# Kernel optimization log

Hardware: AMD Instinct MI355X
Metric: run time of the kernel (lower is better)

## Reference

```python
import jax, jax.numpy as jnp
import numpy as np

# Emformer config (from torchaudio.models.Emformer in BasicNet4)
D, H, FFN, L = 512, 4, 128, 4      # input_dim, num_heads, ffn_dim, num_layers
SEG, RC = 4, 1                     # segment_length, right_context_length
B, T = 8, 1025
U = T - RC                         # utterance length = 1024
NSEG = -(-U // SEG)                # 256 segments
R = NSEG * RC                      # total right-context frames = 256
DH = D // H


def _right_context_indices():
    # torchaudio _gen_right_context: segment i's right context = frames [(i+1)*SEG : (i+1)*SEG+RC],
    # last block = input[T-RC:]
    idx = [np.arange((i + 1) * SEG, (i + 1) * SEG + RC) for i in range(NSEG - 1)]
    idx.append(np.arange(T - RC, T))
    return np.concatenate(idx)


def _attention_mask():
    # Rows / cols ordered [right-context blocks (seg order), utterance frames].
    # A query belonging to segment i may attend to segment i's right-context block
    # and segment i's utterance frames (left_context_length=0, no memory bank).
    seg_rc = np.repeat(np.arange(NSEG), RC)
    seg_u = np.arange(U) // SEG
    seg_q = np.concatenate([seg_rc, seg_u])
    seg_k = np.concatenate([seg_rc, seg_u])
    return seg_q[:, None] == seg_k[None, :]  # (R+U, R+U), True = allowed


def _ln(x, g, b, eps=1e-5):
    mu = jnp.mean(x, -1, keepdims=True)
    var = jnp.mean(jnp.square(x - mu), -1, keepdims=True)
    return (x - mu) * jax.lax.rsqrt(var + eps) * g + b


def setup_inputs() -> dict:
    key = jax.random.key(0)
    ks = jax.random.split(key, 8)
    s = 0.02
    return {
        "x": jax.random.normal(ks[0], (B, T, D), jnp.float32),
        "Wq": jax.random.normal(ks[1], (L, D, D), jnp.float32) * s,
        "bq": jnp.zeros((L, D), jnp.float32),
        "Wkv": jax.random.normal(ks[2], (L, 2 * D, D), jnp.float32) * s,
        "bkv": jnp.zeros((L, 2 * D), jnp.float32),
        "Wo": jax.random.normal(ks[3], (L, D, D), jnp.float32) * s,
        "bo": jnp.zeros((L, D), jnp.float32),
        "W1": jax.random.normal(ks[4], (L, FFN, D), jnp.float32) * s,
        "b1": jnp.zeros((L, FFN), jnp.float32),
        "W2": jax.random.normal(ks[5], (L, D, FFN), jnp.float32) * s,
        "b2": jnp.zeros((L, D), jnp.float32),
        "ln_in_g": jnp.ones((L, D), jnp.float32),
        "ln_in_b": jnp.zeros((L, D), jnp.float32),
        "ff_ln_g": jnp.ones((L, D), jnp.float32),
        "ff_ln_b": jnp.zeros((L, D), jnp.float32),
        "ln_out_g": jnp.ones((L, D), jnp.float32),
        "ln_out_b": jnp.zeros((L, D), jnp.float32),
    }


def reference(x, Wq, bq, Wkv, bkv, Wo, bo, W1, b1, W2, b2,
              ln_in_g, ln_in_b, ff_ln_g, ff_ln_b, ln_out_g, ln_out_b):
    rc_idx = jnp.asarray(_right_context_indices())
    allowed = jnp.asarray(_attention_mask())
    scale = DH ** -0.5
    u = x[:, :U]          # (B, U, D) utterance
    r = x[:, rc_idx]      # (B, R, D) gathered right-context blocks
    for l in range(L):
        cat = jnp.concatenate([r, u], axis=1)            # (B, R+U, D)
        ln = _ln(cat, ln_in_g[l], ln_in_b[l])            # pre-attention LN
        q = (ln @ Wq[l].T + bq[l]).reshape(B, R + U, H, DH)
        kv = ln @ Wkv[l].T + bkv[l]
        k = kv[..., :D].reshape(B, R + U, H, DH)
        v = kv[..., D:].reshape(B, R + U, H, DH)
        scores = jnp.einsum("bqhd,bkhd->bhqk", q * scale, k)
        scores = jnp.where(allowed, scores, -jnp.inf)
        probs = jax.nn.softmax(scores, axis=-1)
        attn = jnp.einsum("bhqk,bkhd->bqhd", probs, v).reshape(B, R + U, D)
        rc_out = attn @ Wo[l].T + bo[l] + cat            # residual w/ pre-LN input
        h = _ln(rc_out, ff_ln_g[l], ff_ln_b[l])
        h = jax.nn.relu(h @ W1[l].T + b1[l]) @ W2[l].T + b2[l]
        rc_out = _ln(rc_out + h, ln_out_g[l], ln_out_b[l])
        r, u = rc_out[:, :R], rc_out[:, R:]
    return u.mean(axis=1)  # (B, D): mean-pool over utterance frames
```

## Files before the change

### kernel.cpp

```cpp
#include <hip/hip_runtime.h>
#include <cstdint>
#include <cstddef>

#define D_    512
#define H_    4
#define DH_   128
#define FFN_  128
#define L_    4
#define B_    8
#define T_    1025
#define U_    1024
#define NSEG_ 256
#define R_    256
#define TOT_  1280
#define M_    (B_*TOT_)
#define CH_   1536

typedef __attribute__((ext_vector_type(8))) short bf16x8;
typedef __attribute__((ext_vector_type(4))) float f32x4;
typedef unsigned short u16;

__device__ __forceinline__ u16 f2bf(float f) {
  unsigned u = __builtin_bit_cast(unsigned, f);
  u += 0x7fff + ((u >> 16) & 1);
  return (u16)(u >> 16);
}
__device__ __forceinline__ float bf2f(u16 h) {
  unsigned u = ((unsigned)h) << 16;
  return __builtin_bit_cast(float, u);
}

__device__ __forceinline__ void gload_lds16(const void* g, void* l) {
  __builtin_amdgcn_global_load_lds(
      (const __attribute__((address_space(1))) unsigned*)g,
      (__attribute__((address_space(3))) unsigned*)l, 16, 0, 0);
}

__global__ __launch_bounds__(256)
void cvt_all_k(const float* __restrict__ Wq, const float* __restrict__ Wkv,
               const float* __restrict__ Wo, const float* __restrict__ W1,
               const float* __restrict__ W2, const float* __restrict__ bq,
               const float* __restrict__ bkv,
               u16* __restrict__ WQKVb, u16* __restrict__ Wob,
               u16* __restrict__ W1b, u16* __restrict__ W2b,
               float* __restrict__ bQKV) {
  int i4 = blockIdx.x * 256 + threadIdx.x;
  if (i4 < 786432) {
    int e = i4 * 4;
    int l = e / 786432;
    int rem = e - l * 786432;
    int n = rem >> 9, k = rem & 511;
    const float* src = (n < 512) ? (Wq + (size_t)l * 262144 + n * 512 + k)
                                 : (Wkv + (size_t)l * 524288 + (n - 512) * 512 + k);
    float4 v = *(const float4*)src;
    ushort4 o; o.x = f2bf(v.x); o.y = f2bf(v.y); o.z = f2bf(v.z); o.w = f2bf(v.w);
    *(ushort4*)(WQKVb + e) = o;
  } else if (i4 < 1048576) {
    int e = (i4 - 786432) * 4;
    float4 v = *(const float4*)(Wo + e);
    ushort4 o; o.x = f2bf(v.x); o.y = f2bf(v.y); o.z = f2bf(v.z); o.w = f2bf(v.w);
    *(ushort4*)(Wob + e) = o;
  } else if (i4 < 1114112) {
    int e = (i4 - 1048576) * 4;
    float4 v = *(const float4*)(W1 + e);
    ushort4 o; o.x = f2bf(v.x); o.y = f2bf(v.y); o.z = f2bf(v.z); o.w = f2bf(v.w);
    *(ushort4*)(W1b + e) = o;
  } else if (i4 < 1179648) {
    int e = (i4 - 1114112) * 4;
    float4 v = *(const float4*)(W2 + e);
    ushort4 o; o.x = f2bf(v.x); o.y = f2bf(v.y); o.z = f2bf(v.z); o.w = f2bf(v.w);
    *(ushort4*)(W2b + e) = o;
  } else if (i4 < 1181184) {
    int e = (i4 - 1179648) * 4;
    int l = e / 1536, n = e - l * 1536;
#pragma unroll
    for (int t = 0; t < 4; ++t) {
      int nn = n + t;
      bQKV[e + t] = (nn < 512) ? bq[l * 512 + nn] : bkv[l * 1024 + (nn - 512)];
    }
  }
}

__global__ __launch_bounds__(256)
void gather_ln_k(const float* __restrict__ x, const float* __restrict__ g,
                 const float* __restrict__ bb, float* __restrict__ X,
                 u16* __restrict__ LNb) {
  int row = blockIdx.x;
  int tid = threadIdx.x;
  int b = row / TOT_, p = row % TOT_;
  int t = (p < R_) ? ((p < R_ - 1) ? 4 * (p + 1) : (T_ - 1)) : (p - R_);
  const float* xr = x + ((size_t)b * T_ + t) * D_;
  float e0 = xr[tid], e1 = xr[tid + 256];
  X[(size_t)row * D_ + tid] = e0;
  X[(size_t)row * D_ + tid + 256] = e1;
  float s = e0 + e1, ss = e0 * e0 + e1 * e1;
#pragma unroll
  for (int off = 32; off > 0; off >>= 1) {
    s  += __shfl_down(s, off);
    ss += __shfl_down(ss, off);
  }
  __shared__ float red[10];
  int wid = tid >> 6, lane = tid & 63;
  if (lane == 0) { red[wid] = s; red[4 + wid] = ss; }
  __syncthreads();
  if (tid == 0) {
    float S = red[0] + red[1] + red[2] + red[3];
    float SS = red[4] + red[5] + red[6] + red[7];
    float mu = S * (1.0f / D_);
    float var = SS * (1.0f / D_) - mu * mu;
    if (var < 0.f) var = 0.f;
    red[8] = mu; red[9] = rsqrtf(var + 1e-5f);
  }
  __syncthreads();
  float mu = red[8], rs = red[9];
  u16* yr = LNb + (size_t)row * D_;
  yr[tid]       = f2bf((e0 - mu) * rs * g[tid]       + bb[tid]);
  yr[tid + 256] = f2bf((e1 - mu) * rs * g[tid + 256] + bb[tid + 256]);
}

#define GBK 32

__global__ __launch_bounds__(256)
void gemm_qkv(const u16* __restrict__ A, const u16* __restrict__ Bw,
              const float* __restrict__ bias, u16* __restrict__ Cout) {
  __shared__ __align__(16) u16 As[128 * GBK];
  __shared__ __align__(16) u16 Bs[128 * GBK];
  const int tid = threadIdx.x;
  const int wid = tid >> 6;
  const int lane = tid & 63;
  const int bid = blockIdx.x;
  const int xcd = bid & 7;
  const int t = bid >> 3;
  const int cb = t % 12;
  const int rb = xcd * 10 + t / 12;
  const int bm = rb * 128;
  const int bn = cb * 128;
  const int wr = wid >> 1, wc = wid & 1;

  const int srow = tid >> 2;
  const int skoff = (tid & 3) << 3;

  f32x4 acc[4][4] = {};

  const u16* Ag0 = A  + (size_t)(bm + srow)      * D_ + skoff;
  const u16* Ag1 = A  + (size_t)(bm + 64 + srow) * D_ + skoff;
  const u16* Bg0 = Bw + (size_t)(bn + srow)      * D_ + skoff;
  const u16* Bg1 = Bw + (size_t)(bn + 64 + srow) * D_ + skoff;
  u16* AsW0 = &As[(size_t)(wid * 16)      * GBK];
  u16* AsW1 = &As[(size_t)(64 + wid * 16) * GBK];
  u16* BsW0 = &Bs[(size_t)(wid * 16)      * GBK];
  u16* BsW1 = &Bs[(size_t)(64 + wid * 16) * GBK];

  const int lrow = lane & 15;
  const int lko  = (lane >> 4) * 16;

  for (int k0 = 0; k0 < D_; k0 += GBK) {
    __syncthreads();
    gload_lds16(Ag0 + k0, AsW0);
    gload_lds16(Ag1 + k0, AsW1);
    gload_lds16(Bg0 + k0, BsW0);
    gload_lds16(Bg1 + k0, BsW1);
    __syncthreads();

    bf16x8 afrag[4], bfrag[4];
#pragma unroll
    for (int m = 0; m < 4; ++m) {
      int row = wr * 64 + m * 16 + lrow;
      afrag[m] = *(const bf16x8*)((const char*)As + row * (GBK * 2) + lko);
    }
#pragma unroll
    for (int n = 0; n < 4; ++n) {
      int col = wc * 64 + n * 16 + lrow;
      bfrag[n] = *(const bf16x8*)((const char*)Bs + col * (GBK * 2) + lko);
    }
#pragma unroll
    for (int m = 0; m < 4; ++m)
#pragma unroll
      for (int n = 0; n < 4; ++n)
        acc[m][n] = __builtin_amdgcn_mfma_f32_16x16x32_bf16(
            afrag[m], bfrag[n], acc[m][n], 0, 0, 0);
  }

  const int lcol  = lane & 15;
  const int lrow4 = (lane >> 4) * 4;
#pragma unroll
  for (int m = 0; m < 4; ++m) {
    int rowbase = bm + wr * 64 + m * 16 + lrow4;
#pragma unroll
    for (int n = 0; n < 4; ++n) {
      int col = bn + wc * 64 + n * 16 + lcol;
      float bv = bias[col];
#pragma unroll
      for (int j = 0; j < 4; ++j) {
        int row = rowbase + j;
        Cout[(size_t)row * CH_ + col] = f2bf(acc[m][n][j] + bv);
      }
    }
  }
}

template <int MODE>
__global__ __launch_bounds__(256)
void gemm_row_ln(const u16* __restrict__ A, const u16* __restrict__ Bw,
                 const float* __restrict__ bias, const float* __restrict__ Rsd,
                 float* __restrict__ Xout,
                 const float* __restrict__ g1, const float* __restrict__ b1,
                 const float* __restrict__ g2, const float* __restrict__ b2,
                 u16* __restrict__ OutBf, int K) {
  __shared__ __align__(16) u16 As[16 * 32];
  __shared__ __align__(16) u16 Bs[512 * 32];
  __shared__ float wsum[4][16], wss[4][16], mu_s[16], rs_s[16];
  const int tid = threadIdx.x;
  const int wid = tid >> 6, lane = tid & 63;
  const int bm = blockIdx.x * 16;
  const int l4 = lane >> 2;
  const int k8 = (lane & 3) << 3;
  const int lrow = lane & 15;
  const int lko  = (lane >> 4) * 16;

  f32x4 acc[8] = {};

  const u16* Ag = A + (size_t)(bm + l4) * K + k8;

  for (int k0 = 0; k0 < K; k0 += 32) {
    __syncthreads();
    if (wid == 0)
      gload_lds16(Ag + k0, As);
#pragma unroll
    for (int p = 0; p < 8; ++p) {
      int row = wid * 128 + p * 16 + l4;
      gload_lds16(Bw + (size_t)row * K + k0 + k8,
                  (char*)Bs + (wid * 128 + p * 16) * 64);
    }
    __syncthreads();

    bf16x8 af = *(const bf16x8*)((const char*)As + lrow * 64 + lko);
    bf16x8 bf[8];
#pragma unroll
    for (int n = 0; n < 8; ++n)
      bf[n] = *(const bf16x8*)((const char*)Bs + (wid * 128 + n * 16 + lrow) * 64 + lko);
#pragma unroll
    for (int n = 0; n < 8; ++n)
      acc[n] = __builtin_amdgcn_mfma_f32_16x16x32_bf16(af, bf[n], acc[n], 0, 0, 0);
  }

  const int lcol = lane & 15;
  const int lr4 = (lane >> 4) * 4;
#pragma unroll
  for (int n = 0; n < 8; ++n) {
    int col = wid * 128 + n * 16 + lcol;
    float bv = bias[col];
#pragma unroll
    for (int j = 0; j < 4; ++j) {
      int row = bm + lr4 + j;
      float t = acc[n][j] + bv + Rsd[(size_t)row * D_ + col];
      if (MODE == 0) Xout[(size_t)row * D_ + col] = t;
      acc[n][j] = t;
    }
  }

  {
    float s0[4] = {}, s1[4] = {};
#pragma unroll
    for (int n = 0; n < 8; ++n)
#pragma unroll
      for (int j = 0; j < 4; ++j) {
        float v = acc[n][j];
        s0[j] += v; s1[j] += v * v;
      }
#pragma unroll
    for (int off = 1; off < 16; off <<= 1)
#pragma unroll
      for (int j = 0; j < 4; ++j) {
        s0[j] += __shfl_xor(s0[j], off);
        s1[j] += __shfl_xor(s1[j], off);
      }
    if ((lane & 15) == 0) {
#pragma unroll
      for (int j = 0; j < 4; ++j) {
        wsum[wid][lr4 + j] = s0[j]; wss[wid][lr4 + j] = s1[j];
      }
    }
  }
  __syncthreads();
  if (tid < 16) {
    float S  = wsum[0][tid] + wsum[1][tid] + wsum[2][tid] + wsum[3][tid];
    float SS = wss[0][tid] + wss[1][tid] + wss[2][tid] + wss[3][tid];
    float mu = S * (1.0f / D_);
    float var = SS * (1.0f / D_) - mu * mu;
    if (var < 0.f) var = 0.f;
    mu_s[tid] = mu; rs_s[tid] = rsqrtf(var + 1e-5f);
  }
  __syncthreads();

  float gg[8], bv2[8];
#pragma unroll
  for (int n = 0; n < 8; ++n) {
    int col = wid * 128 + n * 16 + lcol;
    gg[n] = g1[col]; bv2[n] = b1[col];
  }
#pragma unroll
  for (int n = 0; n < 8; ++n) {
    int col = wid * 128 + n * 16 + lcol;
#pragma unroll
    for (int j = 0; j < 4; ++j) {
      int r = lr4 + j;
      int row = bm + r;
      float ln = (acc[n][j] - mu_s[r]) * rs_s[r] * gg[n] + bv2[n];
      if (MODE == 0) {
        OutBf[(size_t)row * D_ + col] = f2bf(ln);
      } else {
        Xout[(size_t)row * D_ + col] = ln;
        acc[n][j] = ln;
      }
    }
  }

  if (MODE == 1) {
    __syncthreads();
    {
      float s0[4] = {}, s1[4] = {};
#pragma unroll
      for (int n = 0; n < 8; ++n)
#pragma unroll
        for (int j = 0; j < 4; ++j) {
          float v = acc[n][j];
          s0[j] += v; s1[j] += v * v;
        }
#pragma unroll
      for (int off = 1; off < 16; off <<= 1)
#pragma unroll
        for (int j = 0; j < 4; ++j) {
          s0[j] += __shfl_xor(s0[j], off);
          s1[j] += __shfl_xor(s1[j], off);
        }
      if ((lane & 15) == 0) {
#pragma unroll
        for (int j = 0; j < 4; ++j) {
          wsum[wid][lr4 + j] = s0[j]; wss[wid][lr4 + j] = s1[j];
        }
      }
    }
    __syncthreads();
    if (tid < 16) {
      float S  = wsum[0][tid] + wsum[1][tid] + wsum[2][tid] + wsum[3][tid];
      float SS = wss[0][tid] + wss[1][tid] + wss[2][tid] + wss[3][tid];
      float mu = S * (1.0f / D_);
      float var = SS * (1.0f / D_) - mu * mu;
      if (var < 0.f) var = 0.f;
      mu_s[tid] = mu; rs_s[tid] = rsqrtf(var + 1e-5f);
    }
    __syncthreads();
#pragma unroll
    for (int n = 0; n < 8; ++n) {
      int col = wid * 128 + n * 16 + lcol;
      gg[n] = g2[col]; bv2[n] = b2[col];
    }
#pragma unroll
    for (int n = 0; n < 8; ++n) {
      int col = wid * 128 + n * 16 + lcol;
#pragma unroll
      for (int j = 0; j < 4; ++j) {
        int r = lr4 + j;
        int row = bm + r;
        float ln = (acc[n][j] - mu_s[r]) * rs_s[r] * gg[n] + bv2[n];
        OutBf[(size_t)row * D_ + col] = f2bf(ln);
      }
    }
  }
}

__global__ __launch_bounds__(256)
void gemm_ffn1(const u16* __restrict__ A, const u16* __restrict__ Bw,
               const float* __restrict__ bias, u16* __restrict__ Hout) {
  __shared__ __align__(16) u16 As[16 * 32];
  __shared__ __align__(16) u16 Bs[128 * 32];
  const int tid = threadIdx.x;
  const int wid = tid >> 6, lane = tid & 63;
  const int bm = blockIdx.x * 16;
  const int l4 = lane >> 2;
  const int k8 = (lane & 3) << 3;
  const int lrow = lane & 15;
  const int lko  = (lane >> 4) * 16;

  f32x4 acc[2] = {};
  const u16* Ag = A + (size_t)(bm + l4) * D_ + k8;

  for (int k0 = 0; k0 < D_; k0 += 32) {
    __syncthreads();
    if (wid == 0)
      gload_lds16(Ag + k0, As);
#pragma unroll
    for (int p = 0; p < 2; ++p) {
      int row = wid * 32 + p * 16 + l4;
      gload_lds16(Bw + (size_t)row * D_ + k0 + k8,
                  (char*)Bs + (wid * 32 + p * 16) * 64);
    }
    __syncthreads();
    bf16x8 af = *(const bf16x8*)((const char*)As + lrow * 64 + lko);
    bf16x8 bf[2];
#pragma unroll
    for (int n = 0; n < 2; ++n)
      bf[n] = *(const bf16x8*)((const char*)Bs + (wid * 32 + n * 16 + lrow) * 64 + lko);
#pragma unroll
    for (int n = 0; n < 2; ++n)
      acc[n] = __builtin_amdgcn_mfma_f32_16x16x32_bf16(af, bf[n], acc[n], 0, 0, 0);
  }

  const int lcol = lane & 15;
  const int lr4 = (lane >> 4) * 4;
#pragma unroll
  for (int n = 0; n < 2; ++n) {
    int col = wid * 32 + n * 16 + lcol;
    float bv = bias[col];
#pragma unroll
    for (int j = 0; j < 4; ++j) {
      int row = bm + lr4 + j;
      float v = fmaxf(acc[n][j] + bv, 0.f);
      Hout[(size_t)row * FFN_ + col] = f2bf(v);
    }
  }
}

#define QLD 516
__global__ __launch_bounds__(256)
void attn_k(const u16* __restrict__ QKV, u16* __restrict__ O) {
  int bs = blockIdx.x;
  int b = bs >> 8, s = bs & 255;
  __shared__ float Qs[5][QLD];
  __shared__ float Ks[5][QLD];
  __shared__ float Vs[5][QLD];
  __shared__ float P[H_][5][5];
  int tid = threadIdx.x;
  const float scale = 0.08838834764831845f;
  int rows[5];
  rows[0] = s;
#pragma unroll
  for (int i = 1; i < 5; ++i) rows[i] = R_ + 4 * s + (i - 1);
  for (int idx = tid; idx < 960; idx += 256) {
    int mtx = idx / 320;
    int rem = idx - mtx * 320;
    int i = rem >> 6, c8 = rem & 63;
    size_t base = ((size_t)b * TOT_ + rows[i]) * CH_ + mtx * 512 + c8 * 8;
    bf16x8 v = *(const bf16x8*)(QKV + base);
    float* dst = (mtx == 0) ? &Qs[i][c8 * 8] : (mtx == 1 ? &Ks[i][c8 * 8] : &Vs[i][c8 * 8]);
    if (mtx == 0) {
#pragma unroll
      for (int t = 0; t < 8; ++t) dst[t] = bf2f((u16)v[t]) * scale;
    } else {
#pragma unroll
      for (int t = 0; t < 8; ++t) dst[t] = bf2f((u16)v[t]);
    }
  }
  __syncthreads();
  int h = tid >> 6, lane = tid & 63;
  if (lane < 25) {
    int i = lane / 5, j = lane % 5;
    float sum = 0.f;
    const float* qp = &Qs[i][h * DH_];
    const float* kp = &Ks[j][h * DH_];
#pragma unroll 8
    for (int d = 0; d < DH_; ++d) sum += qp[d] * kp[d];
    P[h][i][j] = sum;
  }
  __syncthreads();
  if (lane < 5) {
    int i = lane;
    float m = P[h][i][0];
#pragma unroll
    for (int j = 1; j < 5; ++j) m = fmaxf(m, P[h][i][j]);
    float e[5], ssum = 0.f;
#pragma unroll
    for (int j = 0; j < 5; ++j) { e[j] = __expf(P[h][i][j] - m); ssum += e[j]; }
    float inv = 1.0f / ssum;
#pragma unroll
    for (int j = 0; j < 5; ++j) P[h][i][j] = e[j] * inv;
  }
  __syncthreads();
  for (int idx = lane; idx < 5 * DH_; idx += 64) {
    int i = idx >> 7, d = idx & (DH_ - 1);
    float o = 0.f;
#pragma unroll
    for (int j = 0; j < 5; ++j) o += P[h][i][j] * Vs[j][h * DH_ + d];
    O[((size_t)b * TOT_ + rows[i]) * D_ + h * DH_ + d] = f2bf(o);
  }
}

__global__ __launch_bounds__(256)
void mean_part_k(const float* __restrict__ X, float* __restrict__ part) {
  int d = blockIdx.x * 256 + threadIdx.x;
  int jc = blockIdx.y;
  int b = blockIdx.z;
  float acc = 0.f;
  const float* base = X + ((size_t)b * TOT_ + R_ + jc * 128) * D_ + d;
  for (int j = 0; j < 128; ++j) acc += base[(size_t)j * D_];
  part[((size_t)b * 8 + jc) * D_ + d] = acc;
}

__global__ __launch_bounds__(256)
void mean_final_k(const float* __restrict__ part, float* __restrict__ out) {
  int i = blockIdx.x * 256 + threadIdx.x;
  int b = i >> 9, d = i & (D_ - 1);
  float acc = 0.f;
#pragma unroll
  for (int c = 0; c < 8; ++c) acc += part[((size_t)b * 8 + c) * D_ + d];
  out[i] = acc * (1.0f / U_);
}

extern "C" void kernel_launch(void* const* d_in, const int* in_sizes, int n_in,
                              void* d_out, int out_size, void* d_ws, size_t ws_size,
                              hipStream_t stream) {
  const float* x      = (const float*)d_in[0];
  const float* Wq     = (const float*)d_in[1];
  const float* bq     = (const float*)d_in[2];
  const float* Wkv    = (const float*)d_in[3];
  const float* bkv    = (const float*)d_in[4];
  const float* Wo     = (const float*)d_in[5];
  const float* bo     = (const float*)d_in[6];
  const float* W1     = (const float*)d_in[7];
  const float* b1     = (const float*)d_in[8];
  const float* W2     = (const float*)d_in[9];
  const float* b2     = (const float*)d_in[10];
  const float* ln_in_g  = (const float*)d_in[11];
  const float* ln_in_b  = (const float*)d_in[12];
  const float* ff_ln_g  = (const float*)d_in[13];
  const float* ff_ln_b  = (const float*)d_in[14];
  const float* ln_out_g = (const float*)d_in[15];
  const float* ln_out_b = (const float*)d_in[16];
  float* out = (float*)d_out;

  char* wsb = (char*)d_ws;
  float* X     = (float*)wsb;
  u16*   LNbuf = (u16*)(wsb + 20971520);
  u16*   QKV   = (u16*)(wsb + 31457280);
  u16*   ATT   = (u16*)(wsb + 62914560);
  u16*   LN2b  = (u16*)(wsb + 73400320);
  u16*   Hb    = (u16*)(wsb + 83886080);
  float* part  = (float*)(wsb + 86507520);
  u16*   WQKVb = (u16*)(wsb + 86638592);
  u16*   Wob   = (u16*)(wsb + 92930048);
  u16*   W1b   = (u16*)(wsb + 95027200);
  u16*   W2b   = (u16*)(wsb + 95551488);
  float* bQKV  = (float*)(wsb + 96075776);

  cvt_all_k<<<4614, 256, 0, stream>>>(Wq, Wkv, Wo, W1, W2, bq, bkv,
                                      WQKVb, Wob, W1b, W2b, bQKV);
  gather_ln_k<<<M_, 256, 0, stream>>>(x, ln_in_g, ln_in_b, X, LNbuf);

  for (int l = 0; l < L_; ++l) {
    const u16* WQKV_l = WQKVb + (size_t)l * CH_ * D_;
    const u16* Wo_l   = Wob   + (size_t)l * D_ * D_;
    const u16* W1_l   = W1b   + (size_t)l * FFN_ * D_;
    const u16* W2_l   = W2b   + (size_t)l * D_ * FFN_;
    const float* bQKV_l = bQKV + (size_t)l * CH_;
    const float* bo_l = bo + (size_t)l * D_;
    const float* b1_l = b1 + (size_t)l * FFN_;
    const float* b2_l = b2 + (size_t)l * D_;

    gemm_qkv<<<960, 256, 0, stream>>>(LNbuf, WQKV_l, bQKV_l, QKV);

    attn_k<<<B_ * NSEG_, 256, 0, stream>>>(QKV, ATT);

    gemm_row_ln<0><<<M_ / 16, 256, 0, stream>>>(
        ATT, Wo_l, bo_l, X, X,
        ff_ln_g + l * D_, ff_ln_b + l * D_, nullptr, nullptr, LN2b, D_);

    gemm_ffn1<<<M_ / 16, 256, 0, stream>>>(LN2b, W1_l, b1_l, Hb);

    if (l < L_ - 1) {
      gemm_row_ln<1><<<M_ / 16, 256, 0, stream>>>(
          Hb, W2_l, b2_l, X, X,
          ln_out_g + l * D_, ln_out_b + l * D_,
          ln_in_g + (l + 1) * D_, ln_in_b + (l + 1) * D_, LNbuf, FFN_);
    } else {
      gemm_row_ln<2><<<M_ / 16, 256, 0, stream>>>(
          Hb, W2_l, b2_l, X, X,
          ln_out_g + l * D_, ln_out_b + l * D_,
          nullptr, nullptr, nullptr, FFN_);
    }
  }

  mean_part_k<<<dim3(2, 8, 8), 256, 0, stream>>>(X, part);
  mean_final_k<<<(B_ * D_) / 256, 256, 0, stream>>>(part, out);
}
```

Measured before the change: 438.6 us.

## Double-buffer LDS tiles and XOR-swizzle layout in QKV GEMM

Gives the QKV projection GEMM two LDS buffers so the global-to-LDS load of the next K tile is issued before the MFMA work on the current tile, and drops one of the two barriers per iteration. It also XOR-swizzles the 16-byte slot each row is stored in and read from, to reduce LDS bank conflicts on fragment reads. LDS use doubles, which may lower occupancy. Correctness relies on the write and read swizzles matching and on the single barrier being enough to order buffer reuse.

Result: no change. 446.3 us (+1.8%).

```diff
diff --git a/kernel.cpp b/kernel.cpp
--- a/kernel.cpp
+++ b/kernel.cpp
@@ -119,12 +119,13 @@
 }
 
 #define GBK 32
+#define QBUF (128 * GBK)
 
 __global__ __launch_bounds__(256)
 void gemm_qkv(const u16* __restrict__ A, const u16* __restrict__ Bw,
               const float* __restrict__ bias, u16* __restrict__ Cout) {
-  __shared__ __align__(16) u16 As[128 * GBK];
-  __shared__ __align__(16) u16 Bs[128 * GBK];
+  __shared__ __align__(16) u16 As[2 * QBUF];
+  __shared__ __align__(16) u16 Bs[2 * QBUF];
   const int tid = threadIdx.x;
   const int wid = tid >> 6;
   const int lane = tid & 63;
@@ -137,8 +138,9 @@
   const int bn = cb * 128;
   const int wr = wid >> 1, wc = wid & 1;
 
-  const int srow = tid >> 2;
-  const int skoff = (tid & 3) << 3;
+  const int srow  = tid >> 2;
+  const int sslot = (tid & 3) ^ ((tid >> 3) & 3);
+  const int skoff = sslot << 3;
 
   f32x4 acc[4][4] = {};
 
@@ -152,26 +154,37 @@
   u16* BsW1 = &Bs[(size_t)(64 + wid * 16) * GBK];
 
   const int lrow = lane & 15;
-  const int lko  = (lane >> 4) * 16;
-
+  const int lko  = (((lane >> 4) ^ ((lrow >> 1) & 3)) << 4);
+
+  gload_lds16(Ag0, AsW0);
+  gload_lds16(Ag1, AsW1);
+  gload_lds16(Bg0, BsW0);
+  gload_lds16(Bg1, BsW1);
+  __syncthreads();
+
+  int cur = 0;
+#pragma unroll 4
   for (int k0 = 0; k0 < D_; k0 += GBK) {
-    __syncthreads();
-    gload_lds16(Ag0 + k0, AsW0);
-    gload_lds16(Ag1 + k0, AsW1);
-    gload_lds16(Bg0 + k0, BsW0);
-    gload_lds16(Bg1 + k0, BsW1);
-    __syncthreads();
-
+    int nxt = cur ^ 1;
+    if (k0 + GBK < D_) {
+      gload_lds16(Ag0 + k0 + GBK, AsW0 + nxt * QBUF);
+      gload_lds16(Ag1 + k0 + GBK, AsW1 + nxt * QBUF);
+      gload_lds16(Bg0 + k0 + GBK, BsW0 + nxt * QBUF);
+      gload_lds16(Bg1 + k0 + GBK, BsW1 + nxt * QBUF);
+    }
+
+    const char* Ab = (const char*)(As + cur * QBUF);
+    const char* Bb = (const char*)(Bs + cur * QBUF);
     bf16x8 afrag[4], bfrag[4];
 #pragma unroll
     for (int m = 0; m < 4; ++m) {
       int row = wr * 64 + m * 16 + lrow;
-      afrag[m] = *(const bf16x8*)((const char*)As + row * (GBK * 2) + lko);
+      afrag[m] = *(const bf16x8*)(Ab + row * (GBK * 2) + lko);
     }
 #pragma unroll
     for (int n = 0; n < 4; ++n) {
       int col = wc * 64 + n * 16 + lrow;
-      bfrag[n] = *(const bf16x8*)((const char*)Bs + col * (GBK * 2) + lko);
+      bfrag[n] = *(const bf16x8*)(Bb + col * (GBK * 2) + lko);
     }
 #pragma unroll
     for (int m = 0; m < 4; ++m)
@@ -179,6 +192,9 @@
       for (int n = 0; n < 4; ++n)
         acc[m][n] = __builtin_amdgcn_mfma_f32_16x16x32_bf16(
             afrag[m], bfrag[n], acc[m][n], 0, 0, 0);
+
+    __syncthreads();
+    cur = nxt;
   }
 
   const int lcol  = lane & 15;
```

## Use 128x128 tiled O-proj GEMM and fuse FF LayerNorm into FFN1

Applied to the files above, without the earlier changes.

Replaces the 16-row, full-width O-projection kernel, which also computed the FF LayerNorm, with a 128x128-tiled GEMM using an XCD-aware block mapping. That kernel adds bias and residual in place into X. The FF LayerNorm moves into the FFN1 kernel: it reads the fp32 X rows, normalises them into a swizzled bf16 LDS tile, then runs the W1 GEMM. This is meant to improve weight reuse in the O-proj GEMM and drop the intermediate LN2 bf16 buffer. The cost is that FFN1 now re-reads the fp32 X and computes the LN statistics with a single-pass variance formula.

After: 400.5 us. 8.7% less time.

```diff
diff --git a/kernel.cpp b/kernel.cpp
--- a/kernel.cpp
+++ b/kernel.cpp
@@ -199,6 +199,175 @@
   }
 }
 
+__global__ __launch_bounds__(256)
+void gemm_oproj(const u16* __restrict__ A, const u16* __restrict__ Bw,
+                const float* __restrict__ bias, float* __restrict__ Xio) {
+  __shared__ __align__(16) u16 As[128 * GBK];
+  __shared__ __align__(16) u16 Bs[128 * GBK];
+  const int tid = threadIdx.x;
+  const int wid = tid >> 6;
+  const int lane = tid & 63;
+  const int bid = blockIdx.x;
+  const int xcd = bid & 7;
+  const int t = bid >> 3;
+  const int cb = t & 3;
+  const int rb = xcd * 10 + (t >> 2);
+  const int bm = rb * 128;
+  const int bn = cb * 128;
+  const int wr = wid >> 1, wc = wid & 1;
+
+  const int srow = tid >> 2;
+  const int skoff = (tid & 3) << 3;
+
+  f32x4 acc[4][4] = {};
+
+  const u16* Ag0 = A  + (size_t)(bm + srow)      * D_ + skoff;
+  const u16* Ag1 = A  + (size_t)(bm + 64 + srow) * D_ + skoff;
+  const u16* Bg0 = Bw + (size_t)(bn + srow)      * D_ + skoff;
+  const u16* Bg1 = Bw + (size_t)(bn + 64 + srow) * D_ + skoff;
+  u16* AsW0 = &As[(size_t)(wid * 16)      * GBK];
+  u16* AsW1 = &As[(size_t)(64 + wid * 16) * GBK];
+  u16* BsW0 = &Bs[(size_t)(wid * 16)      * GBK];
+  u16* BsW1 = &Bs[(size_t)(64 + wid * 16) * GBK];
+
+  const int lrow = lane & 15;
+  const int lko  = (lane >> 4) * 16;
+
+  for (int k0 = 0; k0 < D_; k0 += GBK) {
+    __syncthreads();
+    gload_lds16(Ag0 + k0, AsW0);
+    gload_lds16(Ag1 + k0, AsW1);
+    gload_lds16(Bg0 + k0, BsW0);
+    gload_lds16(Bg1 + k0, BsW1);
+    __syncthreads();
+
+    bf16x8 afrag[4], bfrag[4];
+#pragma unroll
+    for (int m = 0; m < 4; ++m) {
+      int row = wr * 64 + m * 16 + lrow;
+      afrag[m] = *(const bf16x8*)((const char*)As + row * (GBK * 2) + lko);
+    }
+#pragma unroll
+    for (int n = 0; n < 4; ++n) {
+      int col = wc * 64 + n * 16 + lrow;
+      bfrag[n] = *(const bf16x8*)((const char*)Bs + col * (GBK * 2) + lko);
+    }
+#pragma unroll
+    for (int m = 0; m < 4; ++m)
+#pragma unroll
+      for (int n = 0; n < 4; ++n)
+        acc[m][n] = __builtin_amdgcn_mfma_f32_16x16x32_bf16(
+            afrag[m], bfrag[n], acc[m][n], 0, 0, 0);
+  }
+
+  const int lcol  = lane & 15;
+  const int lrow4 = (lane >> 4) * 4;
+#pragma unroll
+  for (int m = 0; m < 4; ++m) {
+    int rowbase = bm + wr * 64 + m * 16 + lrow4;
+#pragma unroll
+    for (int n = 0; n < 4; ++n) {
+      int col = bn + wc * 64 + n * 16 + lcol;
+      float bv = bias[col];
+#pragma unroll
+      for (int j = 0; j < 4; ++j) {
+        size_t idx = (size_t)(rowbase + j) * D_ + col;
+        Xio[idx] = acc[m][n][j] + bv + Xio[idx];
+      }
+    }
+  }
+}
+
+__global__ __launch_bounds__(256)
+void ffn1_ln(const float* __restrict__ X,
+             const float* __restrict__ gff, const float* __restrict__ bff,
+             const u16* __restrict__ W1, const float* __restrict__ b1,
+             u16* __restrict__ Hout) {
+  __shared__ __align__(16) u16 Aln[16 * 512];
+  __shared__ __align__(16) u16 Bs[128 * 32];
+  const int tid = threadIdx.x;
+  const int wid = tid >> 6, lane = tid & 63;
+  const int bm = blockIdx.x * 16;
+  const int r  = tid >> 4;
+  const int jj = tid & 15;
+
+  const float* xr = X + (size_t)(bm + r) * D_ + jj * 32;
+  float v[32];
+  float s = 0.f, ss = 0.f;
+#pragma unroll
+  for (int i = 0; i < 8; ++i) {
+    float4 q = *(const float4*)(xr + i * 4);
+    v[i * 4 + 0] = q.x; v[i * 4 + 1] = q.y;
+    v[i * 4 + 2] = q.z; v[i * 4 + 3] = q.w;
+    s  += q.x + q.y + q.z + q.w;
+    ss += q.x * q.x + q.y * q.y + q.z * q.z + q.w * q.w;
+  }
+#pragma unroll
+  for (int off = 1; off < 16; off <<= 1) {
+    s  += __shfl_xor(s, off);
+    ss += __shfl_xor(ss, off);
+  }
+  float mu = s * (1.0f / D_);
+  float var = ss * (1.0f / D_) - mu * mu;
+  if (var < 0.f) var = 0.f;
+  float rs = rsqrtf(var + 1e-5f);
+
+  char* Ab = (char*)Aln;
+#pragma unroll
+  for (int i = 0; i < 8; ++i) {
+    int c0 = jj * 32 + i * 4;
+    float4 g4 = *(const float4*)(gff + c0);
+    float4 b4 = *(const float4*)(bff + c0);
+    ushort4 o;
+    o.x = f2bf((v[i * 4 + 0] - mu) * rs * g4.x + b4.x);
+    o.y = f2bf((v[i * 4 + 1] - mu) * rs * g4.y + b4.y);
+    o.z = f2bf((v[i * 4 + 2] - mu) * rs * g4.z + b4.z);
+    o.w = f2bf((v[i * 4 + 3] - mu) * rs * g4.w + b4.w);
+    int byteoff = (r * 1024 + c0 * 2) ^ ((r & 7) << 4);
+    *(ushort4*)(Ab + byteoff) = o;
+  }
+  __syncthreads();
+
+  const int lrow = lane & 15;
+  const int lko  = (lane >> 4) << 4;
+  const int l4 = lane >> 2;
+  const int k8 = (lane & 3) << 3;
+  f32x4 acc[2] = {};
+
+  for (int k0 = 0; k0 < D_; k0 += 32) {
+    if (k0) __syncthreads();
+#pragma unroll
+    for (int p = 0; p < 2; ++p) {
+      int rowb = wid * 32 + p * 16 + l4;
+      gload_lds16(W1 + (size_t)rowb * D_ + k0 + k8,
+                  (char*)Bs + (wid * 32 + p * 16) * 64);
+    }
+    __syncthreads();
+    bf16x8 af = *(const bf16x8*)((const char*)Aln +
+                  ((lrow * 1024 + k0 * 2 + lko) ^ ((lrow & 7) << 4)));
+    bf16x8 bf[2];
+#pragma unroll
+    for (int n = 0; n < 2; ++n)
+      bf[n] = *(const bf16x8*)((const char*)Bs + (wid * 32 + n * 16 + lrow) * 64 + lko);
+#pragma unroll
+    for (int n = 0; n < 2; ++n)
+      acc[n] = __builtin_amdgcn_mfma_f32_16x16x32_bf16(af, bf[n], acc[n], 0, 0, 0);
+  }
+
+  const int lcol = lane & 15;
+  const int lr4 = (lane >> 4) * 4;
+#pragma unroll
+  for (int n = 0; n < 2; ++n) {
+    int col = wid * 32 + n * 16 + lcol;
+    float bv = b1[col];
+#pragma unroll
+    for (int j = 0; j < 4; ++j) {
+      int row = bm + lr4 + j;
+      Hout[(size_t)row * FFN_ + col] = f2bf(fmaxf(acc[n][j] + bv, 0.f));
+    }
+  }
+}
+
 template <int MODE>
 __global__ __launch_bounds__(256)
 void gemm_row_ln(const u16* __restrict__ A, const u16* __restrict__ Bw,
@@ -254,7 +423,6 @@
     for (int j = 0; j < 4; ++j) {
       int row = bm + lr4 + j;
       float t = acc[n][j] + bv + Rsd[(size_t)row * D_ + col];
-      if (MODE == 0) Xout[(size_t)row * D_ + col] = t;
       acc[n][j] = t;
     }
   }
@@ -307,12 +475,8 @@
       int r = lr4 + j;
       int row = bm + r;
       float ln = (acc[n][j] - mu_s[r]) * rs_s[r] * gg[n] + bv2[n];
-      if (MODE == 0) {
-        OutBf[(size_t)row * D_ + col] = f2bf(ln);
-      } else {
-        Xout[(size_t)row * D_ + col] = ln;
-        acc[n][j] = ln;
-      }
+      Xout[(size_t)row * D_ + col] = ln;
+      acc[n][j] = ln;
     }
   }
 
@@ -366,58 +530,6 @@
         float ln = (acc[n][j] - mu_s[r]) * rs_s[r] * gg[n] + bv2[n];
         OutBf[(size_t)row * D_ + col] = f2bf(ln);
       }
-    }
-  }
-}
-
-__global__ __launch_bounds__(256)
-void gemm_ffn1(const u16* __restrict__ A, const u16* __restrict__ Bw,
-               const float* __restrict__ bias, u16* __restrict__ Hout) {
-  __shared__ __align__(16) u16 As[16 * 32];
-  __shared__ __align__(16) u16 Bs[128 * 32];
-  const int tid = threadIdx.x;
-  const int wid = tid >> 6, lane = tid & 63;
-  const int bm = blockIdx.x * 16;
-  const int l4 = lane >> 2;
-  const int k8 = (lane & 3) << 3;
-  const int lrow = lane & 15;
-  const int lko  = (lane >> 4) * 16;
-
-  f32x4 acc[2] = {};
-  const u16* Ag = A + (size_t)(bm + l4) * D_ + k8;
-
-  for (int k0 = 0; k0 < D_; k0 += 32) {
-    __syncthreads();
-    if (wid == 0)
-      gload_lds16(Ag + k0, As);
-#pragma unroll
-    for (int p = 0; p < 2; ++p) {
-      int row = wid * 32 + p * 16 + l4;
-      gload_lds16(Bw + (size_t)row * D_ + k0 + k8,
-                  (char*)Bs + (wid * 32 + p * 16) * 64);
-    }
-    __syncthreads();
-    bf16x8 af = *(const bf16x8*)((const char*)As + lrow * 64 + lko);
-    bf16x8 bf[2];
-#pragma unroll
-    for (int n = 0; n < 2; ++n)
-      bf[n] = *(const bf16x8*)((const char*)Bs + (wid * 32 + n * 16 + lrow) * 64 + lko);
-#pragma unroll
-    for (int n = 0; n < 2; ++n)
-      acc[n] = __builtin_amdgcn_mfma_f32_16x16x32_bf16(af, bf[n], acc[n], 0, 0, 0);
-  }
-
-  const int lcol = lane & 15;
-  const int lr4 = (lane >> 4) * 4;
-#pragma unroll
-  for (int n = 0; n < 2; ++n) {
-    int col = wid * 32 + n * 16 + lcol;
-    float bv = bias[col];
-#pragma unroll
-    for (int j = 0; j < 4; ++j) {
-      int row = bm + lr4 + j;
-      float v = fmaxf(acc[n][j] + bv, 0.f);
-      Hout[(size_t)row * FFN_ + col] = f2bf(v);
     }
   }
 }
@@ -534,7 +646,6 @@
   u16*   LNbuf = (u16*)(wsb + 20971520);
   u16*   QKV   = (u16*)(wsb + 31457280);
   u16*   ATT   = (u16*)(wsb + 62914560);
-  u16*   LN2b  = (u16*)(wsb + 73400320);
   u16*   Hb    = (u16*)(wsb + 83886080);
   float* part  = (float*)(wsb + 86507520);
   u16*   WQKVb = (u16*)(wsb + 86638592);
@@ -561,11 +672,10 @@
 
     attn_k<<<B_ * NSEG_, 256, 0, stream>>>(QKV, ATT);
 
-    gemm_row_ln<0><<<M_ / 16, 256, 0, stream>>>(
-        ATT, Wo_l, bo_l, X, X,
-        ff_ln_g + l * D_, ff_ln_b + l * D_, nullptr, nullptr, LN2b, D_);
-
-    gemm_ffn1<<<M_ / 16, 256, 0, stream>>>(LN2b, W1_l, b1_l, Hb);
+    gemm_oproj<<<320, 256, 0, stream>>>(ATT, Wo_l, bo_l, X);
+
+    ffn1_ln<<<M_ / 16, 256, 0, stream>>>(
+        X, ff_ln_g + l * D_, ff_ln_b + l * D_, W1_l, b1_l, Hb);
 
     if (l < L_ - 1) {
       gemm_row_ln<1><<<M_ / 16, 256, 0, stream>>>(
```
